# Kernel tuning notes

Measured on AMD Instinct MI355X. Metric: run time of the kernel, lower is better.

## Reference

```python
import jax, jax.numpy as jnp
import numpy as np

B, L = 4096, 4096

# 16 power-series exponents applied to each of the 4 physical params
PS_POWERS = jnp.array([-5.0, -4.0, -3.0, -2.0, -1.5, -1.0, -0.5, 0.0,
                       0.5, 2.0, 1.0/3.0, 3.0, 0.25, 4.0, 0.2, 5.0], dtype=jnp.float32)
# polynomial exponents of the ansatz y(eta)
POLY_POWERS = jnp.array([2.0, 5.0, 8.0, 11.0, 14.0], dtype=jnp.float32)


def setup_inputs() -> dict:
    key = jax.random.key(0)
    k1, k2, k3, k4, k5, k6 = jax.random.split(key, 6)
    # positive inputs: negative/fractional powers require x > 0
    physical_params = jax.random.uniform(k1, (B, 4), jnp.float32, minval=0.1, maxval=2.0)
    eta = jax.random.uniform(k2, (B, L), jnp.float32, minval=0.1, maxval=2.0)
    # MLP params: Linear(64, 32) and Linear(32, 5), torch layout [out, in]
    W1 = jax.random.normal(k3, (32, 64), jnp.float32) * (1.0 / np.sqrt(64.0))
    b1 = jax.random.normal(k4, (32,), jnp.float32) * 0.05
    W2 = jax.random.normal(k5, (5, 32), jnp.float32) * (1.0 / np.sqrt(32.0))
    b2 = jax.random.normal(k6, (5,), jnp.float32) * 0.05
    return {"physical_params": physical_params, "eta": eta,
            "W1": W1, "b1": b1, "W2": W2, "b2": b2}


def reference(physical_params, eta, W1, b1, W2, b2):
    # power-series transform: [B,4] -> [B,4,16] -> [B,64]
    t = (physical_params[:, :, None] ** PS_POWERS).reshape(physical_params.shape[0], -1)
    # global (scalar) normalization; torch .std() is unbiased (ddof=1)
    mean = t.mean()
    std = jnp.std(t, ddof=1)
    norm = (t - mean) / std
    # network = Sequential(ReLU, Linear(64,32), Linear(32,5)) -- ReLU first, no act between linears
    h = jnp.maximum(norm, 0.0) @ W1.T + b1            # [B, 32]
    coefficients = h @ W2.T + b2                       # [B, 5]
    # dy/deta[i,j] = sum_k c[i,k] * p_k * eta[i,j]^(p_k - 1)  (vectorizes the per-row loop)
    eta_pows = eta[:, :, None] ** (POLY_POWERS - 1.0)  # [B, L, 5]
    dy_deta = jnp.einsum('bk,bjk->bj', coefficients * POLY_POWERS, eta_pows)  # [B, L]
    return dy_deta
```

## Files before the change

### kernel.cpp

```cpp
#include <hip/hip_runtime.h>
#include <math.h>

static constexpr int B  = 4096;
static constexpr int L  = 4096;
static constexpr int NX = B * 4;
static constexpr int STATS_THREADS = 1024;
static constexpr int ROWS_PER_BLK  = 4;

typedef float f4 __attribute__((ext_vector_type(4)));

__device__ __constant__ float c_ps_powers[16] = {
    -5.0f, -4.0f, -3.0f, -2.0f, -1.5f, -1.0f, -0.5f, 0.0f,
     0.5f,  2.0f,  0.33333334f, 3.0f, 0.25f, 4.0f, 0.2f, 5.0f};

__device__ __constant__ float c_poly[5] = {2.0f, 5.0f, 8.0f, 11.0f, 14.0f};

__device__ __forceinline__ float hw_log2(float x) { return __builtin_amdgcn_logf(x); }
__device__ __forceinline__ float hw_exp2(float x) { return __builtin_amdgcn_exp2f(x); }

__global__ __launch_bounds__(STATS_THREADS)
void k_stats(const float* __restrict__ pp, float* __restrict__ stats) {
    const int tid = threadIdx.x;
    const f4* pp4 = reinterpret_cast<const f4*>(pp);
    double s = 0.0, s2 = 0.0;
    #pragma unroll
    for (int k = 0; k < NX / 4 / STATS_THREADS; ++k) {
        const f4 xv = pp4[tid + k * STATS_THREADS];
        #pragma unroll
        for (int c = 0; c < 4; ++c) {
            const float lx = hw_log2(xv[c]);
            float sf = 0.0f, sf2 = 0.0f;
            #pragma unroll
            for (int p = 0; p < 16; ++p) {
                const float t = hw_exp2(c_ps_powers[p] * lx);
                sf  += t;
                sf2 = fmaf(t, t, sf2);
            }
            s  += (double)sf;
            s2 += (double)sf2;
        }
    }
    __shared__ double sh_s[STATS_THREADS];
    __shared__ double sh_s2[STATS_THREADS];
    sh_s[tid] = s; sh_s2[tid] = s2;
    __syncthreads();
    for (int off = STATS_THREADS >> 1; off > 0; off >>= 1) {
        if (tid < off) {
            sh_s[tid]  += sh_s[tid + off];
            sh_s2[tid] += sh_s2[tid + off];
        }
        __syncthreads();
    }
    if (tid == 0) {
        const double n    = (double)(B * 64);
        const double mean = sh_s[0] / n;
        const double var  = (sh_s2[0] - n * mean * mean) / (n - 1.0);
        stats[0] = (float)mean;
        stats[1] = (float)(1.0 / sqrt(var));
    }
}

__device__ __forceinline__ float poly_eval(float e, float c0, float c1,
                                           float c2, float c3, float c4) {
    const float e3 = e * e * e;
    float w   = e;
    float acc = c0 * w;
    w *= e3;
    acc = fmaf(c1, w, acc);
    w *= e3;
    acc = fmaf(c2, w, acc);
    w *= e3;
    acc = fmaf(c3, w, acc);
    w *= e3;
    acc = fmaf(c4, w, acc);
    return acc;
}

__global__ __launch_bounds__(256)
void k_fused(const float* __restrict__ pp,  const float* __restrict__ eta,
             const float* __restrict__ W1,  const float* __restrict__ b1,
             const float* __restrict__ W2,  const float* __restrict__ b2,
             const float* __restrict__ stats, float* __restrict__ out) {
    const int blk = blockIdx.x;
    const int tid = threadIdx.x;
    const int row0 = blk * ROWS_PER_BLK;

    __shared__ float sh_r[ROWS_PER_BLK][64];
    __shared__ float sh_h[ROWS_PER_BLK][32];
    __shared__ float sh_c[ROWS_PER_BLK][8];

    {
        const float mean    = stats[0];
        const float inv_std = stats[1];
        const int r = tid >> 6;
        const int j = tid & 63;
        const float x = pp[(row0 + r) * 4 + (j >> 4)];
        const float t = hw_exp2(c_ps_powers[j & 15] * hw_log2(x));
        sh_r[r][j] = fmaxf((t - mean) * inv_std, 0.0f);
    }
    __syncthreads();

    if (tid < 128) {
        const int r = tid >> 5;
        const int h = tid & 31;
        float acc = b1[h];
        const float* w = W1 + h * 64;
        #pragma unroll
        for (int j = 0; j < 64; ++j) acc = fmaf(sh_r[r][j], w[j], acc);
        sh_h[r][h] = acc;
    }
    __syncthreads();

    if (tid < 32) {
        const int r = tid >> 3;
        const int k = tid & 7;
        if (k < 5) {
            float acc = b2[k];
            const float* w = W2 + k * 32;
            #pragma unroll
            for (int o = 0; o < 32; ++o) acc = fmaf(sh_h[r][o], w[o], acc);
            sh_c[r][k] = acc * c_poly[k];
        }
    }
    __syncthreads();

    #pragma unroll
    for (int rr = 0; rr < ROWS_PER_BLK; ++rr) {
        const float c0 = sh_c[rr][0], c1 = sh_c[rr][1], c2 = sh_c[rr][2],
                    c3 = sh_c[rr][3], c4 = sh_c[rr][4];
        const f4* ep = reinterpret_cast<const f4*>(eta + (size_t)(row0 + rr) * L);
        f4*       op = reinterpret_cast<f4*>(out + (size_t)(row0 + rr) * L);
        #pragma unroll
        for (int it = 0; it < L / 4 / 256; ++it) {
            const int i = tid + it * 256;
            const f4 e = ep[i];
            f4 r;
            r.x = poly_eval(e.x, c0, c1, c2, c3, c4);
            r.y = poly_eval(e.y, c0, c1, c2, c3, c4);
            r.z = poly_eval(e.z, c0, c1, c2, c3, c4);
            r.w = poly_eval(e.w, c0, c1, c2, c3, c4);
            op[i] = r;
        }
    }
}

extern "C" void kernel_launch(void* const* d_in, const int* in_sizes, int n_in,
                              void* d_out, int out_size, void* d_ws, size_t ws_size,
                              hipStream_t stream) {
    const float* pp  = (const float*)d_in[0];
    const float* eta = (const float*)d_in[1];
    const float* W1  = (const float*)d_in[2];
    const float* b1  = (const float*)d_in[3];
    const float* W2  = (const float*)d_in[4];
    const float* b2  = (const float*)d_in[5];
    float* out = (float*)d_out;

    float* stats = (float*)d_ws;

    k_stats<<<1, STATS_THREADS, 0, stream>>>(pp, stats);
    k_fused<<<B / ROWS_PER_BLK, 256, 0, stream>>>(pp, eta, W1, b1, W2, b2,
                                                  stats, out);
}
```

Measured before the change: 41.53 us.

## Merge stats and main kernels into one cooperative kernel with grid sync

After: 83.84 us. 2.02x slower.

```diff
diff --git a/kernel.cpp b/kernel.cpp
--- a/kernel.cpp
+++ b/kernel.cpp
@@ -1,11 +1,13 @@
 #include <hip/hip_runtime.h>
+#include <hip/hip_cooperative_groups.h>
 #include <math.h>
+
+namespace cg = cooperative_groups;
 
 static constexpr int B  = 4096;
 static constexpr int L  = 4096;
-static constexpr int NX = B * 4;
-static constexpr int STATS_THREADS = 1024;
-static constexpr int ROWS_PER_BLK  = 4;
+static constexpr int ROWS_PER_BLK = 4;
+static constexpr int NBLK = B / ROWS_PER_BLK;
 
 typedef float f4 __attribute__((ext_vector_type(4)));
 
@@ -17,48 +19,6 @@
 
 __device__ __forceinline__ float hw_log2(float x) { return __builtin_amdgcn_logf(x); }
 __device__ __forceinline__ float hw_exp2(float x) { return __builtin_amdgcn_exp2f(x); }
-
-__global__ __launch_bounds__(STATS_THREADS)
-void k_stats(const float* __restrict__ pp, float* __restrict__ stats) {
-    const int tid = threadIdx.x;
-    const f4* pp4 = reinterpret_cast<const f4*>(pp);
-    double s = 0.0, s2 = 0.0;
-    #pragma unroll
-    for (int k = 0; k < NX / 4 / STATS_THREADS; ++k) {
-        const f4 xv = pp4[tid + k * STATS_THREADS];
-        #pragma unroll
-        for (int c = 0; c < 4; ++c) {
-            const float lx = hw_log2(xv[c]);
-            float sf = 0.0f, sf2 = 0.0f;
-            #pragma unroll
-            for (int p = 0; p < 16; ++p) {
-                const float t = hw_exp2(c_ps_powers[p] * lx);
-                sf  += t;
-                sf2 = fmaf(t, t, sf2);
-            }
-            s  += (double)sf;
-            s2 += (double)sf2;
-        }
-    }
-    __shared__ double sh_s[STATS_THREADS];
-    __shared__ double sh_s2[STATS_THREADS];
-    sh_s[tid] = s; sh_s2[tid] = s2;
-    __syncthreads();
-    for (int off = STATS_THREADS >> 1; off > 0; off >>= 1) {
-        if (tid < off) {
-            sh_s[tid]  += sh_s[tid + off];
-            sh_s2[tid] += sh_s2[tid + off];
-        }
-        __syncthreads();
-    }
-    if (tid == 0) {
-        const double n    = (double)(B * 64);
-        const double mean = sh_s[0] / n;
-        const double var  = (sh_s2[0] - n * mean * mean) / (n - 1.0);
-        stats[0] = (float)mean;
-        stats[1] = (float)(1.0 / sqrt(var));
-    }
-}
 
 __device__ __forceinline__ float poly_eval(float e, float c0, float c1,
                                            float c2, float c3, float c4) {
@@ -76,22 +36,69 @@
     return acc;
 }
 
-__global__ __launch_bounds__(256)
-void k_fused(const float* __restrict__ pp,  const float* __restrict__ eta,
-             const float* __restrict__ W1,  const float* __restrict__ b1,
-             const float* __restrict__ W2,  const float* __restrict__ b2,
-             const float* __restrict__ stats, float* __restrict__ out) {
+__global__ __launch_bounds__(256, 4)
+void k_all(const float* __restrict__ pp,  const float* __restrict__ eta,
+           const float* __restrict__ W1,  const float* __restrict__ b1,
+           const float* __restrict__ W2,  const float* __restrict__ b2,
+           double* __restrict__ part, float* __restrict__ out) {
+    cg::grid_group grid = cg::this_grid();
+    const int tid = threadIdx.x;
     const int blk = blockIdx.x;
-    const int tid = threadIdx.x;
+
+    __shared__ double sh_s[256];
+    __shared__ double sh_s2[256];
+    __shared__ float  sh_r[ROWS_PER_BLK][64];
+    __shared__ float  sh_h[ROWS_PER_BLK][32];
+    __shared__ float  sh_c[ROWS_PER_BLK][8];
+
+    {
+        const int g = blk * 256 + tid;
+        const float x  = pp[g >> 4];
+        const float t  = hw_exp2(c_ps_powers[g & 15] * hw_log2(x));
+        sh_s[tid]  = (double)t;
+        sh_s2[tid] = (double)t * (double)t;
+    }
+    __syncthreads();
+    for (int off = 128; off > 0; off >>= 1) {
+        if (tid < off) {
+            sh_s[tid]  += sh_s[tid + off];
+            sh_s2[tid] += sh_s2[tid + off];
+        }
+        __syncthreads();
+    }
+    if (tid == 0) {
+        part[blk]        = sh_s[0];
+        part[NBLK + blk] = sh_s2[0];
+    }
+
+    grid.sync();
+
+    {
+        double s = 0.0, s2 = 0.0;
+        #pragma unroll
+        for (int k = 0; k < NBLK / 256; ++k) {
+            s  += part[tid + k * 256];
+            s2 += part[NBLK + tid + k * 256];
+        }
+        sh_s[tid] = s; sh_s2[tid] = s2;
+    }
+    __syncthreads();
+    for (int off = 128; off > 0; off >>= 1) {
+        if (tid < off) {
+            sh_s[tid]  += sh_s[tid + off];
+            sh_s2[tid] += sh_s2[tid + off];
+        }
+        __syncthreads();
+    }
+    const double n      = 262144.0;
+    const double mean_d = sh_s[0] / n;
+    const double var    = (sh_s2[0] - n * mean_d * mean_d) / (n - 1.0);
+    const float  mean    = (float)mean_d;
+    const float  inv_std = (float)(1.0 / sqrt(var));
+
     const int row0 = blk * ROWS_PER_BLK;
 
-    __shared__ float sh_r[ROWS_PER_BLK][64];
-    __shared__ float sh_h[ROWS_PER_BLK][32];
-    __shared__ float sh_c[ROWS_PER_BLK][8];
-
     {
-        const float mean    = stats[0];
-        const float inv_std = stats[1];
         const int r = tid >> 6;
         const int j = tid & 63;
         const float x = pp[(row0 + r) * 4 + (j >> 4)];
@@ -153,11 +160,11 @@
     const float* b1  = (const float*)d_in[3];
     const float* W2  = (const float*)d_in[4];
     const float* b2  = (const float*)d_in[5];
-    float* out = (float*)d_out;
+    float* out   = (float*)d_out;
+    double* part = (double*)d_ws;
 
-    float* stats = (float*)d_ws;
-
-    k_stats<<<1, STATS_THREADS, 0, stream>>>(pp, stats);
-    k_fused<<<B / ROWS_PER_BLK, 256, 0, stream>>>(pp, eta, W1, b1, W2, b2,
-                                                  stats, out);
+    void* args[] = {(void*)&pp, (void*)&eta, (void*)&W1, (void*)&b1,
+                    (void*)&W2, (void*)&b2, (void*)&part, (void*)&out};
+    hipLaunchCooperativeKernel((const void*)k_all, dim3(NBLK), dim3(256),
+                               args, 0, stream);
 }
```
